# Optimization experiments

Hardware: AMD Instinct MI355X
Metric: run time of the kernel (lower is better)

The kernel has to match this reference:

```python
import jax, jax.numpy as jnp
import numpy as np

N = 50000
E = 800000
NODE_F = 128
HID = 96
TEMP_F = 10


def setup_inputs() -> dict:
    key = jax.random.key(0)
    ks = jax.random.split(key, 10)
    x = jax.random.normal(ks[0], (N, NODE_F), dtype=jnp.float32)
    edge_index = jax.random.randint(ks[1], (2, E), 0, N, dtype=jnp.int64)
    temporal = jax.random.normal(ks[2], (N, TEMP_F), dtype=jnp.float32)
    # GCNConv: lin weight [in, out] (no bias in lin), separate bias [out]
    W_gcn = jax.random.normal(ks[3], (NODE_F, HID), dtype=jnp.float32) / np.sqrt(NODE_F)
    b_gcn = jnp.zeros((HID,), dtype=jnp.float32)
    W1 = jax.random.normal(ks[4], (HID + TEMP_F, HID), dtype=jnp.float32) / np.sqrt(HID + TEMP_F)
    b1 = jax.random.normal(ks[5], (HID,), dtype=jnp.float32) * 0.01
    W2 = jax.random.normal(ks[6], (HID + NODE_F, 1), dtype=jnp.float32) / np.sqrt(HID + NODE_F)
    b2 = jax.random.normal(ks[7], (1,), dtype=jnp.float32) * 0.01
    return {"x": x, "edge_index": edge_index, "temporal": temporal,
            "W_gcn": W_gcn, "b_gcn": b_gcn, "W1": W1, "b1": b1, "W2": W2, "b2": b2}


def _gcn_conv(x, edge_index, W, b):
    n = x.shape[0]
    loop = jnp.arange(n, dtype=edge_index.dtype)
    src = jnp.concatenate([edge_index[0], loop])  # [E+N]
    dst = jnp.concatenate([edge_index[1], loop])
    # symmetric normalization with self-loops (PyG gcn_norm)
    ones = jnp.ones(src.shape[0], dtype=x.dtype)
    deg = jax.ops.segment_sum(ones, dst, num_segments=n)
    dinv = jnp.where(deg > 0, jax.lax.rsqrt(deg), 0.0)
    norm = dinv[src] * dinv[dst]  # [E+N]
    h = x @ W  # [N, HID]
    msg = h[src] * norm[:, None]  # [E+N, HID] gather + scale
    out = jax.ops.segment_sum(msg, dst, num_segments=n)  # scatter-add
    return out + b


def reference(x, edge_index, temporal, W_gcn, b_gcn, W1, b1, W2, b2):
    h = jax.nn.relu(_gcn_conv(x, edge_index, W_gcn, b_gcn))  # [N, HID]
    h = jnp.concatenate([h, temporal], axis=-1)              # [N, HID+TEMP_F]
    h = jax.nn.relu(h @ W1 + b1)                             # [N, HID]
    h = jnp.concatenate([h, x], axis=-1)                     # [N, HID+NODE_F]
    return jax.nn.relu(h @ W2 + b2)                          # [N, 1]
```

## Files before the change

kernel.cpp:

```cpp
#include <hip/hip_runtime.h>
#include <hip/hip_bf16.h>

#define NN 50000
#define NPAD 50048
#define NE 800000
#define NF 128
#define HH 96
#define TF 10
#define Z1DIM (HH + TF)
#define ZK 128
#define NCH 4
#define CW 24
#define NBK 196
#define CAP 5120
#define EPB 4096
#define FILLA_B ((NE + EPB - 1) / EPB)

typedef __attribute__((ext_vector_type(8))) short short8;
typedef __attribute__((ext_vector_type(8))) unsigned short ushort8;
typedef __attribute__((ext_vector_type(4))) float f32x4;

__device__ __forceinline__ float bu2f(unsigned short u) {
    union { unsigned int i; float f; } c;
    c.i = ((unsigned int)u) << 16;
    return c.f;
}
__device__ __forceinline__ unsigned short f2bu(float f) {
    union { __hip_bfloat16 h; unsigned short u; } c;
    c.h = __float2bfloat16(f);
    return c.u;
}

__global__ void k_init(int* __restrict__ bcur, int* __restrict__ off,
                       int* __restrict__ deg) {
    int i = blockIdx.x * 256 + threadIdx.x;
    if (i < NN) deg[i] = 0;
    if (i < NBK) bcur[i] = i * CAP;
    if (i == NN) off[NN] = NE;
}

#define WBLK (NF * HH / 4 / 256)
#define W1BLK (HH * ZK / 4 / 256)
#define ZTBLK (NPAD / 32)
#define ZPBLK 5
__global__ __launch_bounds__(256) void k_pre(const int* __restrict__ ei,
                                             int* __restrict__ bcur,
                                             int* __restrict__ temp,
                                             int* __restrict__ deg,
                                             const float* __restrict__ W,
                                             const float* __restrict__ W1,
                                             const float* __restrict__ tmp,
                                             unsigned short* __restrict__ Wt,
                                             unsigned short* __restrict__ Wt1,
                                             unsigned short* __restrict__ zb) {
    const int t = threadIdx.x;
    if (blockIdx.x < FILLA_B) {
        __shared__ int hist[NBK], bas[NBK];
        for (int m = t; m < NBK; m += 256) hist[m] = 0;
        __syncthreads();
        const int e0 = blockIdx.x * EPB;
        const int ecap = min(e0 + EPB, NE);
        for (int e = e0 + t; e < ecap; e += 256) {
            int d = ei[NE + e];
            atomicAdd(&hist[d >> 8], 1);
            atomicAdd(&deg[d], 1);
        }
        __syncthreads();
        for (int m = t; m < NBK; m += 256) {
            int c = hist[m];
            bas[m] = c ? atomicAdd(&bcur[m], c) : 0;
            hist[m] = 0;
        }
        __syncthreads();
        for (int e = e0 + t; e < ecap; e += 256) {
            int d = ei[NE + e], s = ei[e];
            int b = d >> 8;
            int r = atomicAdd(&hist[b], 1);
            temp[bas[b] + r] = ((d & 255) << 16) | s;
        }
        return;
    }
    int b = blockIdx.x - FILLA_B;
    if (b < WBLK) {
        int e = (b * 256 + t) * 4;
        int n = e >> 7, k = e & 127;
        ushort4 v;
        v.x = f2bu(W[(k + 0) * HH + n]);
        v.y = f2bu(W[(k + 1) * HH + n]);
        v.z = f2bu(W[(k + 2) * HH + n]);
        v.w = f2bu(W[(k + 3) * HH + n]);
        *(ushort4*)(Wt + e) = v;
    } else if (b < WBLK + W1BLK) {
        int e = ((b - WBLK) * 256 + t) * 4;
        int n = e >> 7, k = e & 127;
        ushort4 v;
        v.x = (k + 0 < Z1DIM) ? f2bu(W1[(k + 0) * HH + n]) : (unsigned short)0;
        v.y = (k + 1 < Z1DIM) ? f2bu(W1[(k + 1) * HH + n]) : (unsigned short)0;
        v.z = (k + 2 < Z1DIM) ? f2bu(W1[(k + 2) * HH + n]) : (unsigned short)0;
        v.w = (k + 3 < Z1DIM) ? f2bu(W1[(k + 3) * HH + n]) : (unsigned short)0;
        *(ushort4*)(Wt1 + e) = v;
    } else if (b < WBLK + W1BLK + ZTBLK) {
        int t4 = ((b - WBLK - W1BLK) * 256 + t) * 4;
        int i = t4 >> 5, cc = t4 & 31;
        ushort4 v; v.x = v.y = v.z = v.w = 0;
        if (i < NN) {
            if (cc + 0 < TF) v.x = f2bu(tmp[(size_t)i * TF + cc + 0]);
            if (cc + 1 < TF) v.y = f2bu(tmp[(size_t)i * TF + cc + 1]);
            if (cc + 2 < TF) v.z = f2bu(tmp[(size_t)i * TF + cc + 2]);
            if (cc + 3 < TF) v.w = f2bu(tmp[(size_t)i * TF + cc + 3]);
        }
        *(ushort4*)(zb + (size_t)i * ZK + HH + cc) = v;
    } else {
        int t4 = ((b - WBLK - W1BLK - ZTBLK) * 256 + t) * 4;
        if (t4 < (NPAD - NN) * HH) {
            int i = NN + t4 / HH, j = t4 % HH;
            ushort4 z; z.x = z.y = z.z = z.w = 0;
            *(ushort4*)(zb + (size_t)i * ZK + j) = z;
        }
    }
}

__global__ __launch_bounds__(256) void k_gg(const int* __restrict__ temp,
                                            const int* __restrict__ bcur,
                                            unsigned short* __restrict__ csr,
                                            int* __restrict__ off,
                                            const float* __restrict__ x,
                                            const unsigned short* __restrict__ Wt,
                                            const float* __restrict__ W2,
                                            const int* __restrict__ deg,
                                            unsigned short* __restrict__ hp_c,
                                            float* __restrict__ xw2) {
    const int t = threadIdx.x;
    if (blockIdx.x < NBK) {
        __shared__ int ls[256], lc[256];
        const int b = blockIdx.x;
        int szt = (t < NBK) ? (bcur[t] - t * CAP) : 0;
        ls[t] = szt;
        __syncthreads();
#pragma unroll
        for (int d = 1; d < 256; d <<= 1) {
            int u = (t >= d) ? ls[t - d] : 0;
            __syncthreads();
            ls[t] += u;
            __syncthreads();
        }
        const int g0 = (b > 0) ? ls[b - 1] : 0;
        __syncthreads();
        ls[t] = 0;
        __syncthreads();
        const int seg0 = b * CAP;
        const int m = bcur[b] - seg0;
        for (int k = t; k < m; k += 256) atomicAdd(&ls[temp[seg0 + k] >> 16], 1);
        __syncthreads();
        const int myc = ls[t];
        lc[t] = myc;
        __syncthreads();
#pragma unroll
        for (int d = 1; d < 256; d <<= 1) {
            int u = (t >= d) ? lc[t - d] : 0;
            __syncthreads();
            lc[t] += u;
            __syncthreads();
        }
        const int myoff = lc[t] - myc;
        __syncthreads();
        lc[t] = myoff;
        const int i = b * 256 + t;
        if (i < NN) off[i] = g0 + myoff;
        __syncthreads();
        for (int k = t; k < m; k += 256) {
            int v = temp[seg0 + k];
            int r = atomicAdd(&lc[v >> 16], 1);
            csr[g0 + r] = (unsigned short)(v & 0xFFFF);
        }
        return;
    }
    const int wave = t >> 6;
    const int lane = t & 63;
    const int quad = lane >> 4;
    const int l16 = lane & 15;
    const int Mbase = (blockIdx.x - NBK) * 64 + wave * 16;
    const int row = Mbase + l16;
    const bool valid = row < NN;

    const float* xr = x + (size_t)row * NF + quad * 8;
    const unsigned short* brow = Wt + (size_t)l16 * NF + quad * 8;

    f32x4 acc[6] = {};
    float xs = 0.f;
#pragma unroll
    for (int ks = 0; ks < 4; ++ks) {
        short8 a = {};
        if (valid) {
            float4 f0 = *(const float4*)(xr + ks * 32);
            float4 f1 = *(const float4*)(xr + ks * 32 + 4);
            const float4 w0 = *(const float4*)(W2 + HH + quad * 8 + ks * 32);
            const float4 w1 = *(const float4*)(W2 + HH + quad * 8 + ks * 32 + 4);
            xs = fmaf(f0.x, w0.x, xs); xs = fmaf(f0.y, w0.y, xs);
            xs = fmaf(f0.z, w0.z, xs); xs = fmaf(f0.w, w0.w, xs);
            xs = fmaf(f1.x, w1.x, xs); xs = fmaf(f1.y, w1.y, xs);
            xs = fmaf(f1.z, w1.z, xs); xs = fmaf(f1.w, w1.w, xs);
            a[0] = (short)f2bu(f0.x); a[1] = (short)f2bu(f0.y);
            a[2] = (short)f2bu(f0.z); a[3] = (short)f2bu(f0.w);
            a[4] = (short)f2bu(f1.x); a[5] = (short)f2bu(f1.y);
            a[6] = (short)f2bu(f1.z); a[7] = (short)f2bu(f1.w);
        }
#pragma unroll
        for (int nt = 0; nt < 6; ++nt) {
            short8 bfrag = *(const short8*)(brow + (size_t)nt * 16 * NF + ks * 32);
            acc[nt] = __builtin_amdgcn_mfma_f32_16x16x32_bf16(a, bfrag, acc[nt], 0, 0, 0);
        }
    }
    xs += __shfl_xor(xs, 16, 64);
    xs += __shfl_xor(xs, 32, 64);
    if (quad == 0 && valid) xw2[row] = xs;

    const int r0 = Mbase + quad * 4;
    float dv[4];
#pragma unroll
    for (int k = 0; k < 4; ++k) {
        int r = r0 + k;
        dv[k] = (r < NN) ? rsqrtf((float)deg[r] + 1.f) : 0.f;
    }
#pragma unroll
    for (int nt = 0; nt < 6; ++nt) {
        int n = nt * 16 + l16;
        int c = n / CW, jj = n - c * CW;
        unsigned short* dst = hp_c + (size_t)c * NN * CW + jj;
#pragma unroll
        for (int k = 0; k < 4; ++k)
            if (r0 + k < NN) dst[(size_t)(r0 + k) * CW] = f2bu(acc[nt][k] * dv[k]);
    }
}

#define RPC2 196
#define AGGB (8 * RPC2)
__global__ __launch_bounds__(256) void k_agg(const unsigned short* __restrict__ hp_c,
                                             const int* __restrict__ off,
                                             const unsigned short* __restrict__ csr,
                                             const float* __restrict__ bg,
                                             unsigned short* __restrict__ zb) {
    const int b = blockIdx.x;
    const int slot = b & 7;
    const int c = slot >> 1;
    const int r = (b >> 3) * 2 + (slot & 1);
    const int item = r * 256 + threadIdx.x;
    if (item >= NN * 2) return;
    const int i = item >> 1;
    const int h = item & 1;
    const unsigned short* __restrict__ base = hp_c + (size_t)c * NN * CW;

    float a[CW];
    if (h == 0) {
        const unsigned short* sp = base + (size_t)i * CW;
        ushort8 s0 = *(const ushort8*)(sp);
        ushort8 s1 = *(const ushort8*)(sp + 8);
        ushort8 s2 = *(const ushort8*)(sp + 16);
#pragma unroll
        for (int j = 0; j < 8; ++j) {
            a[j] = bu2f(s0[j]); a[8 + j] = bu2f(s1[j]); a[16 + j] = bu2f(s2[j]);
        }
    } else {
#pragma unroll
        for (int j = 0; j < CW; ++j) a[j] = 0.f;
    }

    const int start = off[i];
    const int end = off[i + 1];
    const int len = end - start;
    const float dv = rsqrtf((float)len + 1.f);
    const int half0 = (len + 1) >> 1;
    int k = h ? start + half0 : start;
    const int ke = h ? end : start + half0;
    for (; k + 1 < ke; k += 2) {
        const unsigned short* p0 = base + (size_t)csr[k] * CW;
        const unsigned short* p1 = base + (size_t)csr[k + 1] * CW;
        ushort8 v0 = *(const ushort8*)(p0);
        ushort8 v1 = *(const ushort8*)(p0 + 8);
        ushort8 v2 = *(const ushort8*)(p0 + 16);
        ushort8 w0 = *(const ushort8*)(p1);
        ushort8 w1 = *(const ushort8*)(p1 + 8);
        ushort8 w2 = *(const ushort8*)(p1 + 16);
#pragma unroll
        for (int j = 0; j < 8; ++j) {
            a[j]      += bu2f(v0[j]) + bu2f(w0[j]);
            a[8 + j]  += bu2f(v1[j]) + bu2f(w1[j]);
            a[16 + j] += bu2f(v2[j]) + bu2f(w2[j]);
        }
    }
    if (k < ke) {
        const unsigned short* p0 = base + (size_t)csr[k] * CW;
        ushort8 v0 = *(const ushort8*)(p0);
        ushort8 v1 = *(const ushort8*)(p0 + 8);
        ushort8 v2 = *(const ushort8*)(p0 + 16);
#pragma unroll
        for (int j = 0; j < 8; ++j) {
            a[j] += bu2f(v0[j]); a[8 + j] += bu2f(v1[j]); a[16 + j] += bu2f(v2[j]);
        }
    }
#pragma unroll
    for (int j = 0; j < CW; ++j) a[j] += __shfl_xor(a[j], 1, 64);
    if (h == 0) {
        const int j0 = c * CW;
        ushort8 o0, o1, o2;
#pragma unroll
        for (int j = 0; j < 8; ++j) {
            o0[j] = f2bu(fmaxf(fmaf(dv, a[j],      bg[j0 + j]),      0.f));
            o1[j] = f2bu(fmaxf(fmaf(dv, a[8 + j],  bg[j0 + 8 + j]),  0.f));
            o2[j] = f2bu(fmaxf(fmaf(dv, a[16 + j], bg[j0 + 16 + j]), 0.f));
        }
        unsigned short* zp = zb + (size_t)i * ZK + j0;
        *(ushort8*)(zp) = o0;
        *(ushort8*)(zp + 8) = o1;
        *(ushort8*)(zp + 16) = o2;
    }
}

__global__ __launch_bounds__(256) void k_mlp2(const unsigned short* __restrict__ zb,
                                              const unsigned short* __restrict__ Wt1,
                                              const float* __restrict__ b1,
                                              const float* __restrict__ W2,
                                              const float* __restrict__ b2,
                                              const float* __restrict__ xw2,
                                              float* __restrict__ out) {
    const int wave = threadIdx.x >> 6;
    const int lane = threadIdx.x & 63;
    const int quad = lane >> 4;
    const int l16 = lane & 15;
    const int Mbase = blockIdx.x * 64 + wave * 16;

    const unsigned short* arow = zb + (size_t)(Mbase + l16) * ZK + quad * 8;
    const unsigned short* brow = Wt1 + (size_t)l16 * ZK + quad * 8;

    f32x4 acc[6] = {};
#pragma unroll
    for (int ks = 0; ks < 4; ++ks) {
        short8 a = *(const short8*)(arow + ks * 32);
#pragma unroll
        for (int nt = 0; nt < 6; ++nt) {
            short8 bfrag = *(const short8*)(brow + (size_t)nt * 16 * ZK + ks * 32);
            acc[nt] = __builtin_amdgcn_mfma_f32_16x16x32_bf16(a, bfrag, acc[nt], 0, 0, 0);
        }
    }
    float bb[6], wa[6];
#pragma unroll
    for (int nt = 0; nt < 6; ++nt) {
        int c = nt * 16 + l16;
        bb[nt] = b1[c];
        wa[nt] = W2[c];
    }
    const float bias2 = b2[0];

#pragma unroll
    for (int reg = 0; reg < 4; ++reg) {
        const int r = Mbase + quad * 4 + reg;
        float p = 0.f;
#pragma unroll
        for (int nt = 0; nt < 6; ++nt)
            p = fmaf(fmaxf(acc[nt][reg] + bb[nt], 0.f), wa[nt], p);
#pragma unroll
        for (int m = 1; m < 16; m <<= 1) p += __shfl_xor(p, m, 64);
        if (l16 == 0 && r < NN) out[r] = fmaxf(p + xw2[r] + bias2, 0.f);
    }
}

extern "C" void kernel_launch(void* const* d_in, const int* in_sizes, int n_in,
                              void* d_out, int out_size, void* d_ws, size_t ws_size,
                              hipStream_t stream) {
    const float* x   = (const float*)d_in[0];
    const int*   ei  = (const int*)d_in[1];
    const float* tmp = (const float*)d_in[2];
    const float* Wg  = (const float*)d_in[3];
    const float* bg  = (const float*)d_in[4];
    const float* W1  = (const float*)d_in[5];
    const float* b1  = (const float*)d_in[6];
    const float* W2  = (const float*)d_in[7];
    const float* b2  = (const float*)d_in[8];
    float* out = (float*)d_out;

    char* base = (char*)d_ws;
    int* off  = (int*)base;
    int* bcur = (int*)(base + (256 << 10));
    int* deg  = (int*)(base + (260 << 10));
    unsigned short* csr = (unsigned short*)(base + (512 << 10));
    unsigned short* Wt  = (unsigned short*)(base + ((size_t)3 << 20));
    unsigned short* Wt1 = Wt + NF * HH;
    unsigned short* hp_c = (unsigned short*)(base + ((size_t)4 << 20));
    unsigned short* zb  = (unsigned short*)(base + ((size_t)14 << 20));
    float* xw2 = (float*)(base + ((size_t)27 << 20));
    int* temp  = (int*)(base + ((size_t)28 << 20));

    k_init <<<(NN + 256) / 256, 256, 0, stream>>>(bcur, off, deg);
    k_pre  <<<FILLA_B + WBLK + W1BLK + ZTBLK + ZPBLK, 256, 0, stream>>>(
                ei, bcur, temp, deg, Wg, W1, tmp, Wt, Wt1, zb);
    k_gg   <<<NBK + NPAD / 64, 256, 0, stream>>>(temp, bcur, csr, off, x, Wt, W2, deg, hp_c, xw2);
    k_agg  <<<AGGB, 256, 0, stream>>>(hp_c, off, csr, bg, zb);
    k_mlp2 <<<NPAD / 64, 256, 0, stream>>>(zb, Wt1, b1, W2, b2, xw2, out);
}
```

Baseline: 197.9 us.

## Derive node degrees from CSR offsets instead of global degree atomics

Removes the per-edge global atomicAdd on a degree array and the 50k-entry degree zeroing. Degree is now computed as off[r+1]-off[r] from the CSR offsets. Offset computation moves out of k_gg into a new k_off kernel so the GEMM blocks can read the offsets, and k_init shrinks to one block. This adds one kernel launch and one extra pass over the bucketed edges in exchange for eliminating 800k contended global atomics.

```diff
diff --git a/kernel.cpp b/kernel.cpp
--- a/kernel.cpp
+++ b/kernel.cpp
@@ -31,12 +31,10 @@
     return c.u;
 }
 
-__global__ void k_init(int* __restrict__ bcur, int* __restrict__ off,
-                       int* __restrict__ deg) {
-    int i = blockIdx.x * 256 + threadIdx.x;
-    if (i < NN) deg[i] = 0;
-    if (i < NBK) bcur[i] = i * CAP;
-    if (i == NN) off[NN] = NE;
+__global__ void k_init(int* __restrict__ bcur, int* __restrict__ off) {
+    int t = threadIdx.x;
+    if (t < NBK) bcur[t] = t * CAP;
+    if (t == 255) off[NN] = NE;
 }
 
 #define WBLK (NF * HH / 4 / 256)
@@ -46,7 +44,6 @@
 __global__ __launch_bounds__(256) void k_pre(const int* __restrict__ ei,
                                              int* __restrict__ bcur,
                                              int* __restrict__ temp,
-                                             int* __restrict__ deg,
                                              const float* __restrict__ W,
                                              const float* __restrict__ W1,
                                              const float* __restrict__ tmp,
@@ -63,7 +60,6 @@
         for (int e = e0 + t; e < ecap; e += 256) {
             int d = ei[NE + e];
             atomicAdd(&hist[d >> 8], 1);
-            atomicAdd(&deg[d], 1);
         }
         __syncthreads();
         for (int m = t; m < NBK; m += 256) {
@@ -120,58 +116,65 @@
     }
 }
 
+__global__ __launch_bounds__(256) void k_off(const int* __restrict__ temp,
+                                             const int* __restrict__ bcur,
+                                             int* __restrict__ off) {
+    __shared__ int ls[256], lc[256];
+    const int b = blockIdx.x, t = threadIdx.x;
+    int szt = (t < NBK) ? (bcur[t] - t * CAP) : 0;
+    ls[t] = szt;
+    __syncthreads();
+#pragma unroll
+    for (int d = 1; d < 256; d <<= 1) {
+        int u = (t >= d) ? ls[t - d] : 0;
+        __syncthreads();
+        ls[t] += u;
+        __syncthreads();
+    }
+    const int g0 = (b > 0) ? ls[b - 1] : 0;
+    __syncthreads();
+    ls[t] = 0;
+    __syncthreads();
+    const int seg0 = b * CAP;
+    const int m = bcur[b] - seg0;
+    for (int k = t; k < m; k += 256) atomicAdd(&ls[temp[seg0 + k] >> 16], 1);
+    __syncthreads();
+    const int myc = ls[t];
+    lc[t] = myc;
+    __syncthreads();
+#pragma unroll
+    for (int d = 1; d < 256; d <<= 1) {
+        int u = (t >= d) ? lc[t - d] : 0;
+        __syncthreads();
+        lc[t] += u;
+        __syncthreads();
+    }
+    const int i = b * 256 + t;
+    if (i < NN) off[i] = g0 + lc[t] - myc;
+}
+
 __global__ __launch_bounds__(256) void k_gg(const int* __restrict__ temp,
                                             const int* __restrict__ bcur,
                                             unsigned short* __restrict__ csr,
-                                            int* __restrict__ off,
+                                            const int* __restrict__ off,
                                             const float* __restrict__ x,
                                             const unsigned short* __restrict__ Wt,
                                             const float* __restrict__ W2,
-                                            const int* __restrict__ deg,
                                             unsigned short* __restrict__ hp_c,
                                             float* __restrict__ xw2) {
     const int t = threadIdx.x;
     if (blockIdx.x < NBK) {
-        __shared__ int ls[256], lc[256];
+        __shared__ int lc[256];
         const int b = blockIdx.x;
-        int szt = (t < NBK) ? (bcur[t] - t * CAP) : 0;
-        ls[t] = szt;
-        __syncthreads();
-#pragma unroll
-        for (int d = 1; d < 256; d <<= 1) {
-            int u = (t >= d) ? ls[t - d] : 0;
-            __syncthreads();
-            ls[t] += u;
-            __syncthreads();
-        }
-        const int g0 = (b > 0) ? ls[b - 1] : 0;
-        __syncthreads();
-        ls[t] = 0;
+        const int i = b * 256 + t;
+        lc[t] = (i < NN) ? off[i] : 0;
         __syncthreads();
         const int seg0 = b * CAP;
         const int m = bcur[b] - seg0;
-        for (int k = t; k < m; k += 256) atomicAdd(&ls[temp[seg0 + k] >> 16], 1);
-        __syncthreads();
-        const int myc = ls[t];
-        lc[t] = myc;
-        __syncthreads();
-#pragma unroll
-        for (int d = 1; d < 256; d <<= 1) {
-            int u = (t >= d) ? lc[t - d] : 0;
-            __syncthreads();
-            lc[t] += u;
-            __syncthreads();
-        }
-        const int myoff = lc[t] - myc;
-        __syncthreads();
-        lc[t] = myoff;
-        const int i = b * 256 + t;
-        if (i < NN) off[i] = g0 + myoff;
-        __syncthreads();
         for (int k = t; k < m; k += 256) {
             int v = temp[seg0 + k];
             int r = atomicAdd(&lc[v >> 16], 1);
-            csr[g0 + r] = (unsigned short)(v & 0xFFFF);
+            csr[r] = (unsigned short)(v & 0xFFFF);
         }
         return;
     }
@@ -220,7 +223,7 @@
 #pragma unroll
     for (int k = 0; k < 4; ++k) {
         int r = r0 + k;
-        dv[k] = (r < NN) ? rsqrtf((float)deg[r] + 1.f) : 0.f;
+        dv[k] = (r < NN) ? rsqrtf((float)(off[r + 1] - off[r]) + 1.f) : 0.f;
     }
 #pragma unroll
     for (int nt = 0; nt < 6; ++nt) {
@@ -381,7 +384,6 @@
     char* base = (char*)d_ws;
     int* off  = (int*)base;
     int* bcur = (int*)(base + (256 << 10));
-    int* deg  = (int*)(base + (260 << 10));
     unsigned short* csr = (unsigned short*)(base + (512 << 10));
     unsigned short* Wt  = (unsigned short*)(base + ((size_t)3 << 20));
     unsigned short* Wt1 = Wt + NF * HH;
@@ -390,10 +392,11 @@
     float* xw2 = (float*)(base + ((size_t)27 << 20));
     int* temp  = (int*)(base + ((size_t)28 << 20));
 
-    k_init <<<(NN + 256) / 256, 256, 0, stream>>>(bcur, off, deg);
+    k_init <<<1, 256, 0, stream>>>(bcur, off);
     k_pre  <<<FILLA_B + WBLK + W1BLK + ZTBLK + ZPBLK, 256, 0, stream>>>(
-                ei, bcur, temp, deg, Wg, W1, tmp, Wt, Wt1, zb);
-    k_gg   <<<NBK + NPAD / 64, 256, 0, stream>>>(temp, bcur, csr, off, x, Wt, W2, deg, hp_c, xw2);
+                ei, bcur, temp, Wg, W1, tmp, Wt, Wt1, zb);
+    k_off  <<<NBK, 256, 0, stream>>>(temp, bcur, off);
+    k_gg   <<<NBK + NPAD / 64, 256, 0, stream>>>(temp, bcur, csr, off, x, Wt, W2, hp_c, xw2);
     k_agg  <<<AGGB, 256, 0, stream>>>(hp_c, off, csr, bg, zb);
     k_mlp2 <<<NPAD / 64, 256, 0, stream>>>(zb, Wt1, b1, W2, b2, xw2, out);
 }
```

New measurement: 174.0 us. 1.14x faster.
